# Optimization experiments

Hardware: AMD Instinct MI355X
Metric: run time of the kernel (lower is better)

## Reference

```python
import math
import jax, jax.numpy as jnp
import numpy as np

B, A, E_IN = 2048, 32, 160   # batch, n_agents, obs dim
H = 128                      # rnn_hidden_dim
NACT = 32                    # n_actions
HE = 256                     # hypernet_embed
G = 3                        # group_num
TAU = 1.0


def setup_inputs() -> dict:
    key = jax.random.key(0)
    ks = iter(jax.random.split(key, 32))
    def w(shape, scale=0.05):
        return (jax.random.normal(next(ks), shape, dtype=jnp.float32) * scale)
    inp = {
        'inputs': jax.random.normal(next(ks), (B, A, E_IN), dtype=jnp.float32),
        'hidden_state': jnp.zeros((B, A, H), dtype=jnp.float32),
        # fc1
        'fc1_w': w((E_IN, H)), 'fc1_b': w((H,)),
        # GRUCell (torch gate order: r, z, n)
        'gru_wi': w((H, 3 * H)), 'gru_wh': w((H, 3 * H)),
        'gru_bi': w((3 * H,)), 'gru_bh': w((3 * H,)),
        # attention projections (no bias)
        'attn_q_w': w((H, H)), 'attn_k_w': w((H, H)),
        # struct_encoder: Linear(A+2 -> HE) ReLU Linear(HE -> HE) Tanh
        'se1_w': w((A + 2, HE)), 'se1_b': w((HE,)),
        'se2_w': w((HE, HE)), 'se2_b': w((HE,)),
        # group_assign
        'ga_w': w((HE, G)), 'ga_b': w((G,)),
        # group embeddings (th.randn * 0.1)
        'group_emb': w((G, HE), scale=0.1),
        # group_decoder: Linear ReLU Linear Tanh
        'gd1_w': w((HE, HE)), 'gd1_b': w((HE,)),
        'gd2_w': w((HE, HE)), 'gd2_b': w((HE,)),
        # hyper_b / hyper_w
        'hb_w': w((HE, NACT)), 'hb_b': w((NACT,)),
        'hw_w': w((HE, H * NACT)), 'hw_b': w((H * NACT,)),
    }
    return inp


def reference(inputs, hidden_state, fc1_w, fc1_b, gru_wi, gru_wh, gru_bi, gru_bh,
              attn_q_w, attn_k_w, se1_w, se1_b, se2_w, se2_b, ga_w, ga_b,
              group_emb, gd1_w, gd1_b, gd2_w, gd2_b, hb_w, hb_b, hw_w, hw_b):
    b, a, e = inputs.shape
    x = jax.nn.relu(inputs.reshape(-1, e) @ fc1_w + fc1_b)          # [b*a, H]
    h_in = hidden_state.reshape(-1, H)
    # torch GRUCell
    gi = x @ gru_wi + gru_bi
    gh = h_in @ gru_wh + gru_bh
    i_r, i_z, i_n = jnp.split(gi, 3, axis=-1)
    h_r, h_z, h_n = jnp.split(gh, 3, axis=-1)
    r = jax.nn.sigmoid(i_r + h_r)
    z = jax.nn.sigmoid(i_z + h_z)
    n = jnp.tanh(i_n + r * h_n)
    h = ((1.0 - z) * n + z * h_in).reshape(b, a, H)

    # graph_better_struct
    q_ = h @ attn_q_w
    k_ = h @ attn_k_w
    scores = jnp.einsum('bid,bjd->bij', q_, k_) / math.sqrt(H)      # [b,a,a]
    eye = jnp.eye(a, dtype=bool)
    scores = jnp.where(eye[None], -1e9, scores)
    attn = jax.nn.softmax(scores, axis=-1)
    attn = 0.5 * (attn + jnp.swapaxes(attn, 1, 2))
    attn = jnp.where(eye[None], 0.0, attn)
    degree = attn.sum(axis=-1, keepdims=True)                       # [b,a,1]
    attn_c = jnp.clip(attn, 1e-8, None)
    entropy = -(attn_c * jnp.log(attn_c)).sum(axis=-1, keepdims=True)
    struct_input = jnp.concatenate([attn, degree, entropy], axis=-1)  # [b,a,a+2]
    struct_feat = jnp.tanh(jax.nn.relu(struct_input @ se1_w + se1_b) @ se2_w + se2_b)
    logits = (struct_feat @ ga_w + ga_b) / max(TAU, 1e-6)
    probs = jax.nn.softmax(logits, axis=-1)                         # [b,a,G]

    group_emb_ag = probs @ group_emb                                # [b,a,HE]
    group_state = jnp.tanh(jax.nn.relu((struct_feat + group_emb_ag) @ gd1_w + gd1_b) @ gd2_w + gd2_b)

    gs_flat = group_state.reshape(b * a, HE)
    fc2_w = (gs_flat @ hw_w + hw_b).reshape(b, a, H, NACT)          # per-sample weights
    fc2_b = (gs_flat @ hb_w + hb_b).reshape(b, a, NACT)
    q = jnp.einsum('bah,baho->bao', h, fc2_w) + fc2_b               # [b,a,NACT]

    return q, h, group_state, probs, attn
```

## Files before the change

### kernel.cpp

```cpp
#include <hip/hip_runtime.h>
#include <math.h>

#define R_TOTAL 65536

typedef __attribute__((ext_vector_type(8))) short short8_t;
typedef __attribute__((ext_vector_type(4))) short short4_t;
typedef __attribute__((ext_vector_type(4))) float f32x4_t;

__device__ __forceinline__ float frcp_(float x) { return __builtin_amdgcn_rcpf(x); }
__device__ __forceinline__ float fast_sigmoid(float x) { return frcp_(1.f + __expf(-x)); }
__device__ __forceinline__ float fast_tanh(float x) {
  float xc = fminf(fmaxf(x, -15.f), 15.f);
  float t = __expf(2.f * xc);
  return (t - 1.f) * frcp_(t + 1.f);
}

__device__ __forceinline__ short f2bf(float x) {
  unsigned u = __float_as_uint(x);
  u += 0x7fff + ((u >> 16) & 1);
  return (short)(u >> 16);
}
__device__ __forceinline__ float bf2f(short s) {
  return __uint_as_float(((unsigned)(unsigned short)s) << 16);
}

__device__ __forceinline__ void async_cp16(const short* gsrc, short* ldst) {
  __builtin_amdgcn_global_load_lds(
      (const __attribute__((address_space(1))) void*)gsrc,
      (__attribute__((address_space(3))) void*)ldst, 16, 0, 0);
}

__device__ __forceinline__ void load_afrag(const float* p, short8_t& h) {
  float4 u0 = *(const float4*)p;
  float4 u1 = *(const float4*)(p + 4);
  float v[8] = {u0.x, u0.y, u0.z, u0.w, u1.x, u1.y, u1.z, u1.w};
#pragma unroll
  for (int i = 0; i < 8; ++i) h[i] = f2bf(v[i]);
}

#define MFMA(ACC, A, B) ACC = __builtin_amdgcn_mfma_f32_16x16x32_bf16(A, B, ACC, 0, 0, 0)

struct PackSeg {
  const float* W;
  int Ksrc, N, KK, blk0, nblk;
  size_t off;
};
struct PackArgs { PackSeg s[11]; };

__global__ __launch_bounds__(256) void pack_all_kernel(PackArgs a, short* __restrict__ P) {
  const int b = blockIdx.x;
  PackSeg seg = a.s[0];
#pragma unroll
  for (int i = 1; i < 11; ++i)
    if (b >= a.s[i].blk0) seg = a.s[i];
  int p = (b - seg.blk0) * 256 + threadIdx.x;
  int i = p & 7, lane = (p >> 3) & 63, kk = (p >> 9) % seg.KK, ct = p / (seg.KK * 512);
  int e = kk * 32 + (lane >> 4) * 8 + i;
  int c = ct * 16 + (lane & 15);
  float w = (e < seg.Ksrc) ? seg.W[(size_t)e * seg.N + c] : 0.f;
  P[seg.off + p] = f2bf(w);
}

__global__ __launch_bounds__(256, 4) void gru_fused_kernel(
    const float* __restrict__ inputs, const float* __restrict__ Hin,
    const short* __restrict__ Fc1p, const float* __restrict__ fc1b,
    const short* __restrict__ WiP, const short* __restrict__ WhP,
    const float* __restrict__ gbi, const float* __restrict__ gbh,
    float* __restrict__ Hout, short* __restrict__ H16) {
  __shared__ short mid[64 * 128];
  const int tid = threadIdx.x;
  const int wave = tid >> 6, lane = tid & 63;
  const int cl = lane & 15, kg = lane >> 4;
  const int row0g = blockIdx.x * 64 + wave * 16;
  const int row0l = wave * 16;

  {
    short8_t ah1[5];
    {
      const float* ap = inputs + (size_t)(row0g + cl) * 160;
#pragma unroll
      for (int kk = 0; kk < 5; ++kk) load_afrag(ap + kk * 32 + kg * 8, ah1[kk]);
    }
    for (int ct = 0; ct < 8; ++ct) {
      f32x4_t a0 = (f32x4_t){0.f, 0.f, 0.f, 0.f};
#pragma unroll
      for (int kk = 0; kk < 5; ++kk) {
        short8_t b_h = *(const short8_t*)(Fc1p + (((size_t)ct * 5 + kk) * 64 + lane) * 8);
        MFMA(a0, ah1[kk], b_h);
      }
      int col = ct * 16 + cl;
      float bv = fc1b[col];
      int c2hi = (col * 2) & ~15, c2lo = (col * 2) & 15;
#pragma unroll
      for (int j = 0; j < 4; ++j) {
        float v0 = fmaxf(a0[j] + bv, 0.f);
        int r0 = row0l + kg * 4 + j;
        int ad0 = ((r0 * 256 + c2hi) ^ ((r0 & 7) << 4)) + c2lo;
        *(short*)((char*)mid + ad0) = f2bf(v0);
      }
    }
  }
  __syncthreads();

  short8_t xh[4], hh[4];
  {
    int row = row0l + cl;
    const float* hp = Hin + (size_t)(row0g + cl) * 128;
#pragma unroll
    for (int kk = 0; kk < 4; ++kk) {
      int ad = (row * 256 + kk * 64 + kg * 16) ^ ((row & 7) << 4);
      xh[kk] = *(const short8_t*)((const char*)mid + ad);
      load_afrag(hp + kk * 32 + kg * 8, hh[kk]);
    }
  }
#define GLOAD(P, CT) *(const short8_t*)((P) + (((size_t)(CT) * 4 + kk) * 64 + lane) * 8)
  for (int ct = 0; ct < 8; ++ct) {
    f32x4_t aXr = (f32x4_t){0.f, 0.f, 0.f, 0.f}, aXz = aXr, aXn = aXr;
    f32x4_t aHr = aXr, aHz = aXr, aHn = aXr;
#pragma unroll
    for (int kk = 0; kk < 4; ++kk) {
      short8_t b_h;
      b_h = GLOAD(WiP, ct);      MFMA(aXr, xh[kk], b_h);
      b_h = GLOAD(WiP, ct + 8);  MFMA(aXz, xh[kk], b_h);
      b_h = GLOAD(WiP, ct + 16); MFMA(aXn, xh[kk], b_h);
      b_h = GLOAD(WhP, ct);      MFMA(aHr, hh[kk], b_h);
      b_h = GLOAD(WhP, ct + 8);  MFMA(aHz, hh[kk], b_h);
      b_h = GLOAD(WhP, ct + 16); MFMA(aHn, hh[kk], b_h);
    }
    int col = ct * 16 + cl;
    float bir = gbi[col], biz = gbi[128 + col], bin = gbi[256 + col];
    float bhr = gbh[col], bhz = gbh[128 + col], bhn = gbh[256 + col];
#pragma unroll
    for (int j = 0; j < 4; ++j) {
      int row = row0g + kg * 4 + j;
      float rg = fast_sigmoid(aXr[j] + aHr[j] + bir + bhr);
      float zg = fast_sigmoid(aXz[j] + aHz[j] + biz + bhz);
      float ng = fast_tanh(aXn[j] + bin + rg * (aHn[j] + bhn));
      float hv = Hin[(size_t)row * 128 + col];
      float ho = (1.f - zg) * ng + zg * hv;
      Hout[(size_t)row * 128 + col] = ho;
      H16[(size_t)row * 128 + col] = f2bf(ho);
    }
  }
#undef GLOAD
}

__global__ __launch_bounds__(256) void attn_fused_kernel(
    const short* __restrict__ H16, const short* __restrict__ QKp,
    float* __restrict__ attn_out, short* __restrict__ si) {
  __shared__ short qkb[2][32 * 128];
  __shared__ float p[32][33];
  const int b = blockIdx.x;
  const int tid = threadIdx.x;
  const int wave = tid >> 6, lane = tid & 63;
  const int cl = lane & 15, kg = lane >> 4;

  {
    short8_t ahf[2][4];
#pragma unroll
    for (int m = 0; m < 2; ++m) {
      const short* ap = H16 + (size_t)(b * 32 + m * 16 + cl) * 128;
#pragma unroll
      for (int kk = 0; kk < 4; ++kk)
        ahf[m][kk] = *(const short8_t*)(ap + kk * 32 + kg * 8);
    }
    const int proj = wave >> 1;
    const short* Wbase = QKp + (size_t)proj * 16384;
    short* dst = &qkb[proj][0];
#pragma unroll
    for (int ct4 = 0; ct4 < 4; ++ct4) {
      int ct = (wave & 1) * 4 + ct4;
      f32x4_t a0 = (f32x4_t){0.f, 0.f, 0.f, 0.f};
      f32x4_t a1 = (f32x4_t){0.f, 0.f, 0.f, 0.f};
#pragma unroll
      for (int kk = 0; kk < 4; ++kk) {
        short8_t b_h = *(const short8_t*)(Wbase + (((size_t)ct * 4 + kk) * 64 + lane) * 8);
        MFMA(a0, ahf[0][kk], b_h);
        MFMA(a1, ahf[1][kk], b_h);
      }
      int col = ct * 16 + cl;
      int c2hi = (col * 2) & ~15, c2lo = (col * 2) & 15;
#pragma unroll
      for (int j = 0; j < 4; ++j) {
        int r0 = kg * 4 + j;
        int r1 = 16 + kg * 4 + j;
        int ad0 = ((r0 * 256 + c2hi) ^ ((r0 & 7) << 4)) + c2lo;
        int ad1 = ((r1 * 256 + c2hi) ^ ((r1 & 7) << 4)) + c2lo;
        *(short*)((char*)dst + ad0) = f2bf(a0[j]);
        *(short*)((char*)dst + ad1) = f2bf(a1[j]);
      }
    }
  }
  __syncthreads();

  {
    const int mi = wave >> 1, nj = wave & 1;
    short8_t qf[4], kf[4];
    int rq = mi * 16 + cl, rk = nj * 16 + cl;
#pragma unroll
    for (int kk = 0; kk < 4; ++kk) {
      int adq = (rq * 256 + kk * 64 + kg * 16) ^ ((rq & 7) << 4);
      int adk = (rk * 256 + kk * 64 + kg * 16) ^ ((rk & 7) << 4);
      qf[kk] = *(const short8_t*)((const char*)&qkb[0][0] + adq);
      kf[kk] = *(const short8_t*)((const char*)&qkb[1][0] + adk);
    }
    f32x4_t acc = (f32x4_t){0.f, 0.f, 0.f, 0.f};
#pragma unroll
    for (int kk = 0; kk < 4; ++kk) MFMA(acc, qf[kk], kf[kk]);
    const float scale = 0.088388347648318447f;
#pragma unroll
    for (int j = 0; j < 4; ++j) {
      int r = mi * 16 + kg * 4 + j;
      int c = nj * 16 + cl;
      p[r][c] = (r == c) ? -1e9f : acc[j] * scale;
    }
  }
  __syncthreads();

  {
    int row = tid >> 3, g = tid & 7;
    float v[4];
    float mx = -1e30f;
#pragma unroll
    for (int c0 = 0; c0 < 4; ++c0) {
      v[c0] = p[row][g * 4 + c0];
      mx = fmaxf(mx, v[c0]);
    }
#pragma unroll
    for (int off = 1; off < 8; off <<= 1) mx = fmaxf(mx, __shfl_xor(mx, off, 64));
    float s = 0.f;
#pragma unroll
    for (int c0 = 0; c0 < 4; ++c0) {
      v[c0] = __expf(v[c0] - mx);
      s += v[c0];
    }
#pragma unroll
    for (int off = 1; off < 8; off <<= 1) s += __shfl_xor(s, off, 64);
    float inv = frcp_(s);
#pragma unroll
    for (int c0 = 0; c0 < 4; ++c0) p[row][g * 4 + c0] = v[c0] * inv;
  }
  __syncthreads();

  {
    int row = tid >> 3, g = tid & 7;
    float vv[4];
    float d = 0.f, en = 0.f;
#pragma unroll
    for (int c0 = 0; c0 < 4; ++c0) {
      int c = g * 4 + c0;
      float v = (row == c) ? 0.f : 0.5f * (p[row][c] + p[c][row]);
      vv[c0] = v;
      d += v;
      float cc = fmaxf(v, 1e-8f);
      en -= cc * __logf(cc);
      attn_out[(size_t)b * 1024 + row * 32 + c] = v;
    }
#pragma unroll
    for (int off = 1; off < 8; off <<= 1) {
      d += __shfl_xor(d, off, 64);
      en += __shfl_xor(en, off, 64);
    }
    short* srow = si + ((size_t)b * 32 + row) * 64;
#pragma unroll
    for (int c0 = 0; c0 < 4; ++c0) srow[g * 4 + c0] = f2bf(vv[c0]);
    if (g == 0) {
      srow[32] = f2bf(d);
      srow[33] = f2bf(en);
    }
    for (int z = 34 + g; z < 64; z += 8) srow[z] = 0;
  }
}

__global__ __launch_bounds__(256, 4) void se_gd_kernel(
    const short* __restrict__ SI,
    const short* __restrict__ Se1p, const float* __restrict__ se1b,
    const short* __restrict__ Se2p, const float* __restrict__ se2b,
    const float* __restrict__ ga_w, const float* __restrict__ ga_b,
    const float* __restrict__ gemb, float* __restrict__ probs,
    const short* __restrict__ Gd1p, const float* __restrict__ gd1b,
    const short* __restrict__ Gd2p, const float* __restrict__ gd2b,
    float* __restrict__ gs_out, short* __restrict__ gs16) {
  __shared__ short mid[64 * 256];
  const int tid = threadIdx.x;
  const int wave = tid >> 6, lane = tid & 63;
  const int cl = lane & 15, kg = lane >> 4;
  const int row0g = blockIdx.x * 64;
  const int row0l = wave * 16;

  {
    short8_t ah1[2];
    {
      const short* ap = SI + (size_t)(row0g + row0l + cl) * 64;
#pragma unroll
      for (int kk = 0; kk < 2; ++kk)
        ah1[kk] = *(const short8_t*)(ap + kk * 32 + kg * 8);
    }
    for (int ct = 0; ct < 16; ++ct) {
      f32x4_t a0 = (f32x4_t){0.f, 0.f, 0.f, 0.f};
#pragma unroll
      for (int kk = 0; kk < 2; ++kk) {
        short8_t b_h = *(const short8_t*)(Se1p + (((size_t)ct * 2 + kk) * 64 + lane) * 8);
        MFMA(a0, ah1[kk], b_h);
      }
      int col = ct * 16 + cl;
      float bv = se1b[col];
      int c2hi = (col * 2) & ~15, c2lo = (col * 2) & 15;
#pragma unroll
      for (int j = 0; j < 4; ++j) {
        float v0 = fmaxf(a0[j] + bv, 0.f);
        int r0 = row0l + kg * 4 + j;
        int ad0 = ((r0 * 512 + c2hi) ^ ((r0 & 7) << 4)) + c2lo;
        *(short*)((char*)mid + ad0) = f2bf(v0);
      }
    }
  }
  __syncthreads();

  {
    short8_t ah2[8];
    {
      int row = row0l + cl;
#pragma unroll
      for (int kk = 0; kk < 8; ++kk) {
        int ad = (row * 512 + kk * 64 + kg * 16) ^ ((row & 7) << 4);
        ah2[kk] = *(const short8_t*)((const char*)mid + ad);
      }
    }
    __syncthreads();
    for (int ct = 0; ct < 16; ++ct) {
      f32x4_t a0 = (f32x4_t){0.f, 0.f, 0.f, 0.f};
#pragma unroll
      for (int kk = 0; kk < 8; ++kk) {
        short8_t b_h = *(const short8_t*)(Se2p + (((size_t)ct * 8 + kk) * 64 + lane) * 8);
        MFMA(a0, ah2[kk], b_h);
      }
      int col = ct * 16 + cl;
      float bv = se2b[col];
      int c2hi = (col * 2) & ~15, c2lo = (col * 2) & 15;
#pragma unroll
      for (int j = 0; j < 4; ++j) {
        float v0 = fast_tanh(a0[j] + bv);
        int r0 = row0l + kg * 4 + j;
        int ad0 = ((r0 * 512 + c2hi) ^ ((r0 & 7) << 4)) + c2lo;
        *(short*)((char*)mid + ad0) = f2bf(v0);
      }
    }
  }
  __syncthreads();

  short8_t tfr[8];
  {
    short8_t sfr[8];
    float lg[3] = {};
    {
      int row = row0l + cl;
#pragma unroll
      for (int kk = 0; kk < 8; ++kk) {
        int ad = (row * 512 + kk * 64 + kg * 16) ^ ((row & 7) << 4);
        short8_t s = *(const short8_t*)((const char*)mid + ad);
        sfr[kk] = s;
        int e0 = kk * 32 + kg * 8;
#pragma unroll
        for (int i = 0; i < 8; ++i) {
          float v = bf2f(s[i]);
          lg[0] = fmaf(v, ga_w[(e0 + i) * 3 + 0], lg[0]);
          lg[1] = fmaf(v, ga_w[(e0 + i) * 3 + 1], lg[1]);
          lg[2] = fmaf(v, ga_w[(e0 + i) * 3 + 2], lg[2]);
        }
      }
    }
#pragma unroll
    for (int g = 0; g < 3; ++g) {
      lg[g] += __shfl_xor(lg[g], 16, 64);
      lg[g] += __shfl_xor(lg[g], 32, 64);
    }
    float l0 = lg[0] + ga_b[0], l1 = lg[1] + ga_b[1], l2 = lg[2] + ga_b[2];
    float mx = fmaxf(l0, fmaxf(l1, l2));
    float e0 = __expf(l0 - mx), e1 = __expf(l1 - mx), e2 = __expf(l2 - mx);
    float inv = frcp_(e0 + e1 + e2);
    float p0 = e0 * inv, p1 = e1 * inv, p2 = e2 * inv;
    if (kg == 0) {
      size_t r = (size_t)(row0g + row0l + cl) * 3;
      probs[r + 0] = p0;
      probs[r + 1] = p1;
      probs[r + 2] = p2;
    }
#pragma unroll
    for (int kk = 0; kk < 8; ++kk) {
      int e0i = kk * 32 + kg * 8;
      short8_t tf;
#pragma unroll
      for (int i = 0; i < 8; ++i) {
        float tv = bf2f(sfr[kk][i]) + p0 * gemb[e0i + i] +
                   p1 * gemb[256 + e0i + i] + p2 * gemb[512 + e0i + i];
        tf[i] = f2bf(tv);
      }
      tfr[kk] = tf;
    }
  }
  __syncthreads();

  for (int ct = 0; ct < 16; ++ct) {
    f32x4_t a0 = (f32x4_t){0.f, 0.f, 0.f, 0.f};
#pragma unroll
    for (int kk = 0; kk < 8; ++kk) {
      short8_t b_h = *(const short8_t*)(Gd1p + (((size_t)ct * 8 + kk) * 64 + lane) * 8);
      MFMA(a0, tfr[kk], b_h);
    }
    int col = ct * 16 + cl;
    float bv = gd1b[col];
    int c2hi = (col * 2) & ~15, c2lo = (col * 2) & 15;
#pragma unroll
    for (int j = 0; j < 4; ++j) {
      float v0 = fmaxf(a0[j] + bv, 0.f);
      int r0 = row0l + kg * 4 + j;
      int ad0 = ((r0 * 512 + c2hi) ^ ((r0 & 7) << 4)) + c2lo;
      *(short*)((char*)mid + ad0) = f2bf(v0);
    }
  }
  __syncthreads();
  {
    short8_t ah2[8];
    {
      int row = row0l + cl;
#pragma unroll
      for (int kk = 0; kk < 8; ++kk) {
        int ad = (row * 512 + kk * 64 + kg * 16) ^ ((row & 7) << 4);
        ah2[kk] = *(const short8_t*)((const char*)mid + ad);
      }
    }
    for (int ct = 0; ct < 16; ++ct) {
      f32x4_t a0 = (f32x4_t){0.f, 0.f, 0.f, 0.f};
#pragma unroll
      for (int kk = 0; kk < 8; ++kk) {
        short8_t b_h = *(const short8_t*)(Gd2p + (((size_t)ct * 8 + kk) * 64 + lane) * 8);
        MFMA(a0, ah2[kk], b_h);
      }
      int col = ct * 16 + cl;
      float bv = gd2b[col];
#pragma unroll
      for (int j = 0; j < 4; ++j) {
        float v0 = fast_tanh(a0[j] + bv);
        size_t r0 = (size_t)(row0g + row0l + kg * 4 + j) * 256 + col;
        gs_out[r0] = v0;
        gs16[r0] = f2bf(v0);
      }
    }
  }
}

__global__ __launch_bounds__(256, 2) void hyper_q_v12_kernel(
    const short* __restrict__ GS16, const short* __restrict__ H16,
    const short* __restrict__ Wp, const float* __restrict__ hwb,
    float* __restrict__ Qpart) {
  __shared__ short Bh[2][8192];
  __shared__ short h_lds[4][64][68];
  const int tid = threadIdx.x;
  const int wave = tid >> 6, lane = tid & 63;
  const int cl = lane & 15, kg = lane >> 4;
  const int half = blockIdx.x >> 8;
  const int wrow = (blockIdx.x & 255) * 256 + wave * 64;
  const int ct_base = half * 128;

  {
    const short* hp = H16 + (size_t)(wrow + lane) * 128 + half * 64;
#pragma unroll
    for (int c = 0; c < 64; c += 8) {
      short8_t v = *(const short8_t*)(hp + c);
#pragma unroll
      for (int i = 0; i < 8; ++i) h_lds[wave][c + i][lane] = v[i];
    }
  }

  short8_t ah[4][8];
#pragma unroll
  for (int m = 0; m < 4; ++m) {
    const short* ap = GS16 + (size_t)(wrow + m * 16 + cl) * 256;
#pragma unroll
    for (int kk = 0; kk < 8; ++kk) ah[m][kk] = *(const short8_t*)(ap + kk * 32 + kg * 8);
  }

  {
    const short* wp0 = Wp + (size_t)ct_base * 4096;
#pragma unroll
    for (int k = 0; k < 4; ++k)
      async_cp16(wp0 + k * 2048 + tid * 8, &Bh[0][k * 2048 + tid * 8]);
  }
  __syncthreads();

  float qf[4][2][4] = {};
  int cur = 0;

#define COMPUTE_CT(BUFP, OH, WB)                                               \
  {                                                                            \
    f32x4_t acc[4];                                                            \
    _Pragma("unroll")                                                          \
    for (int m = 0; m < 4; ++m) acc[m] = (f32x4_t){(WB), (WB), (WB), (WB)};    \
    _Pragma("unroll")                                                          \
    for (int kk = 0; kk < 8; ++kk) {                                           \
      short8_t b_h = *(const short8_t*)((BUFP) + ((OH) * 4096 + (kk * 64 + lane) * 8)); \
      _Pragma("unroll")                                                        \
      for (int m = 0; m < 4; ++m) MFMA(acc[m], ah[m][kk], b_h);                \
    }                                                                          \
    _Pragma("unroll")                                                          \
    for (int m = 0; m < 4; ++m)                                                \
      _Pragma("unroll")                                                        \
      for (int j = 0; j < 4; ++j)                                              \
        qf[m][OH][j] = fmaf(hc[m * 4 + j], acc[m][j], qf[m][OH][j]);           \
  }

  for (int t2 = 0; t2 < 64; ++t2) {
    const int ct0 = ct_base + t2 * 2;
    if (t2 < 63) {
      const short* wpn = Wp + (size_t)(ct0 + 2) * 4096;
      short* bufn = &Bh[cur ^ 1][0];
#pragma unroll
      for (int k = 0; k < 4; ++k)
        async_cp16(wpn + k * 2048 + tid * 8, bufn + k * 2048 + tid * 8);
    }
    float hc[16];
#pragma unroll
    for (int m = 0; m < 4; ++m) {
      short4_t v4 = *(const short4_t*)&h_lds[wave][t2][m * 16 + kg * 4];
#pragma unroll
      for (int j = 0; j < 4; ++j) hc[m * 4 + j] = bf2f(v4[j]);
    }
    float wb0 = hwb[ct0 * 16 + cl];
    float wb1 = hwb[(ct0 + 1) * 16 + cl];
    const short* bufp = &Bh[cur][0];
    COMPUTE_CT(bufp, 0, wb0)
    COMPUTE_CT(bufp, 1, wb1)
    __syncthreads();
    cur ^= 1;
  }
#undef COMPUTE_CT

  if (half == 0) {
#pragma unroll
    for (int oh = 0; oh < 2; ++oh) {
      f32x4_t bacc[4];
#pragma unroll
      for (int m = 0; m < 4; ++m) bacc[m] = (f32x4_t){0.f, 0.f, 0.f, 0.f};
#pragma unroll
      for (int kk = 0; kk < 8; ++kk) {
        short8_t b_h = *(const short8_t*)(Wp + (((size_t)(256 + oh) * 8 + kk) * 64 + lane) * 8);
#pragma unroll
        for (int m = 0; m < 4; ++m) MFMA(bacc[m], ah[m][kk], b_h);
      }
#pragma unroll
      for (int m = 0; m < 4; ++m)
#pragma unroll
        for (int j = 0; j < 4; ++j) qf[m][oh][j] += bacc[m][j];
    }
  }

  float* qp = Qpart + (size_t)half * 2097152;
#pragma unroll
  for (int m = 0; m < 4; ++m)
#pragma unroll
    for (int j = 0; j < 4; ++j) {
      const size_t r = (size_t)(wrow + m * 16 + kg * 4 + j) * 32;
      qp[r + cl] = qf[m][0][j];
      qp[r + 16 + cl] = qf[m][1][j];
    }
}

__global__ __launch_bounds__(256) void qcombine_kernel(
    const float* __restrict__ Qpart, const float* __restrict__ hbb,
    float* __restrict__ Qout) {
  int i = blockIdx.x * 256 + threadIdx.x;
  float4 a = ((const float4*)Qpart)[i];
  float4 b = ((const float4*)(Qpart + 2097152))[i];
  float4 e = ((const float4*)hbb)[i & 7];
  ((float4*)Qout)[i] = make_float4(a.x + b.x + e.x, a.y + b.y + e.y,
                                   a.z + b.z + e.z, a.w + b.w + e.w);
}

extern "C" void kernel_launch(void* const* d_in, const int* in_sizes, int n_in,
                              void* d_out, int out_size, void* d_ws, size_t ws_size,
                              hipStream_t stream) {
  const float* inputs   = (const float*)d_in[0];
  const float* hidden   = (const float*)d_in[1];
  const float* fc1_w    = (const float*)d_in[2];
  const float* fc1_b    = (const float*)d_in[3];
  const float* gru_wi   = (const float*)d_in[4];
  const float* gru_wh   = (const float*)d_in[5];
  const float* gru_bi   = (const float*)d_in[6];
  const float* gru_bh   = (const float*)d_in[7];
  const float* attn_q_w = (const float*)d_in[8];
  const float* attn_k_w = (const float*)d_in[9];
  const float* se1_w    = (const float*)d_in[10];
  const float* se1_b    = (const float*)d_in[11];
  const float* se2_w    = (const float*)d_in[12];
  const float* se2_b    = (const float*)d_in[13];
  const float* ga_w     = (const float*)d_in[14];
  const float* ga_b     = (const float*)d_in[15];
  const float* gemb     = (const float*)d_in[16];
  const float* gd1_w    = (const float*)d_in[17];
  const float* gd1_b    = (const float*)d_in[18];
  const float* gd2_w    = (const float*)d_in[19];
  const float* gd2_b    = (const float*)d_in[20];
  const float* hb_w     = (const float*)d_in[21];
  const float* hb_b     = (const float*)d_in[22];
  const float* hw_w     = (const float*)d_in[23];
  const float* hw_b     = (const float*)d_in[24];

  float* out = (float*)d_out;
  float* q_out     = out;
  float* h_out     = out + 2097152;
  float* gs_out    = out + 10485760;
  float* probs_out = out + 27262976;
  float* attn_out  = out + 27459584;

  char* wsb = (char*)d_ws;
  float* qpart = (float*)wsb;
  short* si   = (short*)(wsb + (size_t)16 * 1024 * 1024);
  short* gs16 = (short*)(wsb + (size_t)24 * 1024 * 1024);
  short* h16  = (short*)(wsb + (size_t)56 * 1024 * 1024);
  short* P    = (short*)(wsb + (size_t)72 * 1024 * 1024);

  const size_t o_hw  = 0;
  const size_t o_hb  = 1048576;
  const size_t o_fc1 = 1056768;
  const size_t o_wi  = 1077248;
  const size_t o_wh  = 1126400;
  const size_t o_qkq = 1175552;
  const size_t o_qkk = 1191936;
  const size_t o_se1 = 1208320;
  const size_t o_se2 = 1224704;
  const size_t o_gd1 = 1290240;
  const size_t o_gd2 = 1355776;

  PackArgs pa;
  pa.s[0]  = {hw_w,     256, 4096, 8, 0,    4096, o_hw};
  pa.s[1]  = {hb_w,     256, 32,   8, 4096, 32,   o_hb};
  pa.s[2]  = {fc1_w,    160, 128,  5, 4128, 80,   o_fc1};
  pa.s[3]  = {gru_wi,   128, 384,  4, 4208, 192,  o_wi};
  pa.s[4]  = {gru_wh,   128, 384,  4, 4400, 192,  o_wh};
  pa.s[5]  = {attn_q_w, 128, 128,  4, 4592, 64,   o_qkq};
  pa.s[6]  = {attn_k_w, 128, 128,  4, 4656, 64,   o_qkk};
  pa.s[7]  = {se1_w,    34,  256,  2, 4720, 64,   o_se1};
  pa.s[8]  = {se2_w,    256, 256,  8, 4784, 256,  o_se2};
  pa.s[9]  = {gd1_w,    256, 256,  8, 5040, 256,  o_gd1};
  pa.s[10] = {gd2_w,    256, 256,  8, 5296, 256,  o_gd2};

  dim3 blk(256);
  pack_all_kernel<<<5552, blk, 0, stream>>>(pa, P);
  gru_fused_kernel<<<1024, blk, 0, stream>>>(inputs, hidden, P + o_fc1, fc1_b,
                                             P + o_wi, P + o_wh, gru_bi, gru_bh,
                                             h_out, h16);
  attn_fused_kernel<<<2048, blk, 0, stream>>>(h16, P + o_qkq, attn_out, si);
  se_gd_kernel<<<1024, blk, 0, stream>>>(si, P + o_se1, se1_b, P + o_se2, se2_b,
                                         ga_w, ga_b, gemb, probs_out,
                                         P + o_gd1, gd1_b, P + o_gd2, gd2_b,
                                         gs_out, gs16);
  hyper_q_v12_kernel<<<dim3(512), blk, 0, stream>>>(gs16, h16, P + o_hw, hw_b, qpart);
  qcombine_kernel<<<2048, blk, 0, stream>>>(qpart, hb_b, q_out);
}
```

Baseline: 260.1 us.

## Use four-slot single-tile LDS ring with explicit vmcnt waits in hyper_q

Replaces the two-buffer, two-tile-per-iteration weight pipeline in the hypernet Q kernel with a four-slot ring of single 16-column tiles, prefetched two iterations ahead. Each iteration waits with an explicit s_waitcnt vmcnt and a raw s_barrier instead of a trailing __syncthreads, so waves can keep more async copies in flight. The hyper-weight bias is also staged once into LDS rather than read from global memory every iteration. The cost is twice as many barriers overall, and correctness now depends on the hand-tuned vmcnt counts.

Result: slower. 287.2 us (+10.4%).

```diff
diff --git a/kernel.cpp b/kernel.cpp
--- a/kernel.cpp
+++ b/kernel.cpp
@@ -450,12 +450,13 @@
   }
 }
 
-__global__ __launch_bounds__(256, 2) void hyper_q_v12_kernel(
+__global__ __launch_bounds__(256, 2) void hyper_q_v13_kernel(
     const short* __restrict__ GS16, const short* __restrict__ H16,
     const short* __restrict__ Wp, const float* __restrict__ hwb,
     float* __restrict__ Qpart) {
-  __shared__ short Bh[2][8192];
+  __shared__ short Bh[4][4096];
   __shared__ short h_lds[4][64][68];
+  __shared__ float hwb_lds[2048];
   const int tid = threadIdx.x;
   const int wave = tid >> 6, lane = tid & 63;
   const int cl = lane & 15, kg = lane >> 4;
@@ -472,6 +473,7 @@
       for (int i = 0; i < 8; ++i) h_lds[wave][c + i][lane] = v[i];
     }
   }
+  for (int i = tid; i < 2048; i += 256) hwb_lds[i] = hwb[ct_base * 16 + i];
 
   short8_t ah[4][8];
 #pragma unroll
@@ -484,57 +486,55 @@
   {
     const short* wp0 = Wp + (size_t)ct_base * 4096;
 #pragma unroll
-    for (int k = 0; k < 4; ++k)
+    for (int k = 0; k < 2; ++k) {
       async_cp16(wp0 + k * 2048 + tid * 8, &Bh[0][k * 2048 + tid * 8]);
+      async_cp16(wp0 + 4096 + k * 2048 + tid * 8, &Bh[1][k * 2048 + tid * 8]);
+    }
   }
   __syncthreads();
 
   float qf[4][2][4] = {};
-  int cur = 0;
-
-#define COMPUTE_CT(BUFP, OH, WB)                                               \
-  {                                                                            \
-    f32x4_t acc[4];                                                            \
-    _Pragma("unroll")                                                          \
-    for (int m = 0; m < 4; ++m) acc[m] = (f32x4_t){(WB), (WB), (WB), (WB)};    \
-    _Pragma("unroll")                                                          \
-    for (int kk = 0; kk < 8; ++kk) {                                           \
-      short8_t b_h = *(const short8_t*)((BUFP) + ((OH) * 4096 + (kk * 64 + lane) * 8)); \
-      _Pragma("unroll")                                                        \
-      for (int m = 0; m < 4; ++m) MFMA(acc[m], ah[m][kk], b_h);                \
-    }                                                                          \
-    _Pragma("unroll")                                                          \
-    for (int m = 0; m < 4; ++m)                                                \
-      _Pragma("unroll")                                                        \
-      for (int j = 0; j < 4; ++j)                                              \
-        qf[m][OH][j] = fmaf(hc[m * 4 + j], acc[m][j], qf[m][OH][j]);           \
-  }
-
-  for (int t2 = 0; t2 < 64; ++t2) {
-    const int ct0 = ct_base + t2 * 2;
-    if (t2 < 63) {
-      const short* wpn = Wp + (size_t)(ct0 + 2) * 4096;
-      short* bufn = &Bh[cur ^ 1][0];
-#pragma unroll
-      for (int k = 0; k < 4; ++k)
+
+  for (int t = 0; t < 128; ++t) {
+    if (t < 126) {
+      const short* wpn = Wp + (size_t)(ct_base + t + 2) * 4096;
+      short* bufn = &Bh[(t + 2) & 3][0];
+#pragma unroll
+      for (int k = 0; k < 2; ++k)
         async_cp16(wpn + k * 2048 + tid * 8, bufn + k * 2048 + tid * 8);
-    }
+      asm volatile("s_waitcnt vmcnt(4)" ::: "memory");
+    } else if (t == 126) {
+      asm volatile("s_waitcnt vmcnt(2)" ::: "memory");
+    } else {
+      asm volatile("s_waitcnt vmcnt(0)" ::: "memory");
+    }
+    __builtin_amdgcn_s_barrier();
+
     float hc[16];
 #pragma unroll
     for (int m = 0; m < 4; ++m) {
-      short4_t v4 = *(const short4_t*)&h_lds[wave][t2][m * 16 + kg * 4];
+      short4_t v4 = *(const short4_t*)&h_lds[wave][t >> 1][m * 16 + kg * 4];
 #pragma unroll
       for (int j = 0; j < 4; ++j) hc[m * 4 + j] = bf2f(v4[j]);
     }
-    float wb0 = hwb[ct0 * 16 + cl];
-    float wb1 = hwb[(ct0 + 1) * 16 + cl];
-    const short* bufp = &Bh[cur][0];
-    COMPUTE_CT(bufp, 0, wb0)
-    COMPUTE_CT(bufp, 1, wb1)
-    __syncthreads();
-    cur ^= 1;
-  }
-#undef COMPUTE_CT
+    float wb = hwb_lds[t * 16 + cl];
+    const int oh = t & 1;
+    const short* bufp = &Bh[t & 3][0];
+    f32x4_t acc[4];
+#pragma unroll
+    for (int m = 0; m < 4; ++m) acc[m] = (f32x4_t){wb, wb, wb, wb};
+#pragma unroll
+    for (int kk = 0; kk < 8; ++kk) {
+      short8_t b_h = *(const short8_t*)(bufp + (kk * 64 + lane) * 8);
+#pragma unroll
+      for (int m = 0; m < 4; ++m) MFMA(acc[m], ah[m][kk], b_h);
+    }
+#pragma unroll
+    for (int m = 0; m < 4; ++m)
+#pragma unroll
+      for (int j = 0; j < 4; ++j)
+        qf[m][oh][j] = fmaf(hc[m * 4 + j], acc[m][j], qf[m][oh][j]);
+  }
 
   if (half == 0) {
 #pragma unroll
@@ -655,6 +655,6 @@
                                          ga_w, ga_b, gemb, probs_out,
                                          P + o_gd1, gd1_b, P + o_gd2, gd2_b,
                                          gs_out, gs16);
-  hyper_q_v12_kernel<<<dim3(512), blk, 0, stream>>>(gs16, h16, P + o_hw, hw_b, qpart);
+  hyper_q_v13_kernel<<<dim3(512), blk, 0, stream>>>(gs16, h16, P + o_hw, hw_b, qpart);
   qcombine_kernel<<<2048, blk, 0, stream>>>(qpart, hb_b, q_out);
 }
```
